# Optimization experiments

Measured on AMD Instinct MI355X. Metric: run time of the kernel, lower is better.

The kernel has to match this reference:

```python
import jax, jax.numpy as jnp
import numpy as np

B, N, D, H = 4, 4096, 1024, 16
DK = D // H  # 64


def setup_inputs() -> dict:
    key = jax.random.key(0)
    ks = jax.random.split(key, 11)
    s_in = 1.0 / np.sqrt(D)
    s_out = 1.0 / np.sqrt(H * DK)
    return {
        "query": jax.random.normal(ks[0], (B, N, D), jnp.float32),
        "key": jax.random.normal(ks[1], (B, N, D), jnp.float32),
        "value": jax.random.normal(ks[2], (B, N, D), jnp.float32),
        # stacked per-head Linear weights (torch Linear: y = x @ W.T + b)
        "Wq": jax.random.uniform(ks[3], (H, DK, D), jnp.float32, -s_in, s_in),
        "bq": jax.random.uniform(ks[4], (H, DK), jnp.float32, -s_in, s_in),
        "Wk": jax.random.uniform(ks[5], (H, DK, D), jnp.float32, -s_in, s_in),
        "bk": jax.random.uniform(ks[6], (H, DK), jnp.float32, -s_in, s_in),
        "Wv": jax.random.uniform(ks[7], (H, DK, D), jnp.float32, -s_in, s_in),
        "bv": jax.random.uniform(ks[8], (H, DK), jnp.float32, -s_in, s_in),
        "Wo": jax.random.uniform(ks[9], (D, H * DK), jnp.float32, -s_out, s_out),
        "bo": jax.random.uniform(ks[10], (D,), jnp.float32, -s_out, s_out),
    }


def reference(query, key, value, Wq, bq, Wk, bk, Wv, bv, Wo, bo):
    b, n, _ = query.shape
    # batched per-head projections: [b,h,n,d_k]
    q = jnp.einsum('bnd,hkd->bhnk', query, Wq) + bq[None, :, None, :]
    k = jnp.einsum('bnd,hkd->bhnk', key, Wk) + bk[None, :, None, :]
    v = jnp.einsum('bnd,hkd->bhnk', value, Wv) + bv[None, :, None, :]
    # linear dot-product attention (faithful: scale by batch**-0.5)
    q = jax.nn.softmax(q, axis=-1) * (b ** -0.5)
    k = jax.nn.softmax(k, axis=-2)  # softmax over sequence dim
    ctx = jnp.einsum('bhnd,bhne->bhde', k, v)      # [b,h,d_k,d_v]
    attn = jnp.einsum('bhnd,bhde->bhne', q, ctx)   # [b,h,n,d_v]
    # concat heads along last dim: [b,n,h*d_v]
    concat = attn.transpose(0, 2, 1, 3).reshape(b, n, -1)
    return concat @ Wo.T + bo
```

## Files before the change

### kernel.cpp

```cpp
#include <hip/hip_runtime.h>
#include <hip/hip_bf16.h>
#include <stdint.h>

#define B_  4
#define N_  4096
#define D_  1024
#define H_  16
#define DK_ 64
#define M_  (B_ * N_)

typedef __attribute__((ext_vector_type(8))) short  short8;
typedef __attribute__((ext_vector_type(4))) float  f32x4;
typedef __attribute__((ext_vector_type(4))) unsigned int u32x4;

__device__ __forceinline__ uint16_t f2bf(float f) {
  union { float f; uint32_t u; } v; v.f = f;
  uint32_t r = v.u + 0x7FFF + ((v.u >> 16) & 1);
  return (uint16_t)(r >> 16);
}
__device__ __forceinline__ uint32_t f2bf2(float lo, float hi) {
  return (uint32_t)f2bf(lo) | ((uint32_t)f2bf(hi) << 16);
}
__device__ __forceinline__ float bf2f(uint16_t u) {
  union { uint32_t u; float f; } v; v.u = ((uint32_t)u) << 16;
  return v.f;
}

__device__ __forceinline__ void gload_lds16(const void* g, void* l) {
  __builtin_amdgcn_global_load_lds((const __attribute__((address_space(1))) void*)g,
                                   (__attribute__((address_space(3))) void*)l, 16, 0, 0);
}

#define S_BARRIER() __builtin_amdgcn_s_barrier()
#define FENCE_LGKM0() asm volatile("s_waitcnt lgkmcnt(0)" ::: "memory")
#define FENCE_VM4()   asm volatile("s_waitcnt vmcnt(4) lgkmcnt(0)" ::: "memory")
#define FENCE_VM0()   asm volatile("s_waitcnt vmcnt(0) lgkmcnt(0)" ::: "memory")

__global__ __launch_bounds__(256) void pack_bf16_kernel(
    const float* q, const float* k, const float* v,
    const float* wq, const float* wk, const float* wv, const float* wo,
    uint16_t* xq, uint16_t* xk, uint16_t* xv,
    uint16_t* bwq, uint16_t* bwk, uint16_t* bwv, uint16_t* bwo)
{
  const float* src; uint16_t* dst; int count;
  switch (blockIdx.y) {
    case 0: src = q;  dst = xq;  count = M_ * D_; break;
    case 1: src = k;  dst = xk;  count = M_ * D_; break;
    case 2: src = v;  dst = xv;  count = M_ * D_; break;
    case 3: src = wq; dst = bwq; count = D_ * D_; break;
    case 4: src = wk; dst = bwk; count = D_ * D_; break;
    case 5: src = wv; dst = bwv; count = D_ * D_; break;
    default: src = wo; dst = bwo; count = D_ * D_; break;
  }
  int base = blockIdx.x * 16384;
  if (base >= count) return;
  int t = threadIdx.x;
#pragma unroll
  for (int it = 0; it < 8; ++it) {
    int idx = base + it * 2048 + t * 8;
    f32x4 f0 = *(const f32x4*)(src + idx);
    f32x4 f1 = *(const f32x4*)(src + idx + 4);
    u32x4 o;
    o.x = f2bf2(f0.x, f0.y); o.y = f2bf2(f0.z, f0.w);
    o.z = f2bf2(f1.x, f1.y); o.w = f2bf2(f1.z, f1.w);
    *(u32x4*)(dst + idx) = o;
  }
}

template<int EPI>
__device__ __forceinline__ void gemm_epilogue(
    f32x4 (&acc)[8][4], int tid, int l, int lr, int kg, int wr, int wc,
    int brow, int bcol, const float* __restrict__ bias, void* __restrict__ C,
    float* __restrict__ pm, float* __restrict__ ps,
    float* sredm, float* sreds)
{
  if (EPI == 2) {
    float bv[4];
#pragma unroll
    for (int ni = 0; ni < 4; ++ni) bv[ni] = bias[bcol * 256 + wc * 64 + ni * 16 + lr];
#pragma unroll
    for (int mi = 0; mi < 8; ++mi) {
#pragma unroll
      for (int j = 0; j < 4; ++j) {
        float v0 = acc[mi][0][j] + bv[0];
        float v1 = acc[mi][1][j] + bv[1];
        float v2 = acc[mi][2][j] + bv[2];
        float v3 = acc[mi][3][j] + bv[3];
        float m = fmaxf(fmaxf(v0, v1), fmaxf(v2, v3));
#pragma unroll
        for (int o = 1; o < 16; o <<= 1) m = fmaxf(m, __shfl_xor(m, o));
        float p0 = __expf(v0 - m), p1 = __expf(v1 - m);
        float p2 = __expf(v2 - m), p3 = __expf(v3 - m);
        float s = (p0 + p1) + (p2 + p3);
#pragma unroll
        for (int o = 1; o < 16; o <<= 1) s += __shfl_xor(s, o);
        float sc = 0.5f / s;
        int row = brow * 256 + wr * 128 + mi * 16 + kg * 4 + j;
        uint16_t* out = (uint16_t*)C + (size_t)row * D_ + bcol * 256 + wc * 64 + lr;
        out[0]  = f2bf(p0 * sc);
        out[16] = f2bf(p1 * sc);
        out[32] = f2bf(p2 * sc);
        out[48] = f2bf(p3 * sc);
      }
    }
  } else if (EPI == 3) {
#pragma unroll
    for (int ni = 0; ni < 4; ++ni) {
      int coll = wc * 64 + ni * 16 + lr;
      int col = bcol * 256 + coll;
      float bvn = bias[col];
      float vals[8][4];
      float m = -1e30f;
#pragma unroll
      for (int mi = 0; mi < 8; ++mi)
#pragma unroll
        for (int j = 0; j < 4; ++j) {
          float val = acc[mi][ni][j] + bvn;
          vals[mi][j] = val;
          m = fmaxf(m, val);
          int row = brow * 256 + wr * 128 + mi * 16 + kg * 4 + j;
          ((uint16_t*)C)[(size_t)row * D_ + col] = f2bf(val);
        }
      m = fmaxf(m, __shfl_xor(m, 16));
      m = fmaxf(m, __shfl_xor(m, 32));
      float s = 0.f;
#pragma unroll
      for (int mi = 0; mi < 8; ++mi)
#pragma unroll
        for (int j = 0; j < 4; ++j) s += __expf(vals[mi][j] - m);
      s += __shfl_xor(s, 16);
      s += __shfl_xor(s, 32);
      if (l < 16) {
        sredm[wr * 256 + coll] = m;
        sreds[wr * 256 + coll] = s;
      }
    }
    __syncthreads();
    if (tid < 256) {
      float m0 = sredm[tid], m1 = sredm[256 + tid];
      float s0 = sreds[tid], s1 = sreds[256 + tid];
      float m = fmaxf(m0, m1);
      float s = s0 * __expf(m0 - m) + s1 * __expf(m1 - m);
      pm[(size_t)brow * D_ + bcol * 256 + tid] = m;
      ps[(size_t)brow * D_ + bcol * 256 + tid] = s;
    }
  } else {
#pragma unroll
    for (int mi = 0; mi < 8; ++mi) {
#pragma unroll
      for (int ni = 0; ni < 4; ++ni) {
        int col = bcol * 256 + wc * 64 + ni * 16 + lr;
        float bv = bias[col];
#pragma unroll
        for (int j = 0; j < 4; ++j) {
          int row = brow * 256 + wr * 128 + mi * 16 + kg * 4 + j;
          float val = acc[mi][ni][j] + bv;
          if (EPI == 1) ((float*)C)[(size_t)row * D_ + col] = val;
          else          ((uint16_t*)C)[(size_t)row * D_ + col] = f2bf(val);
        }
      }
    }
  }
}

__device__ __forceinline__ void gemm256_body(
    const uint16_t* __restrict__ A, const uint16_t* __restrict__ Wb,
    uint16_t* As, uint16_t* Bs,
    int tid, int w, int arow0, int bcrow0, int srcswz, int rsw,
    int lr, int kg, int wr, int wc, f32x4 (&acc)[8][4])
{
  const int NT = 16;
  const uint16_t* gA[2][2];
  const uint16_t* gB[2][2];
  int lOff[2][2];
#pragma unroll
  for (int h = 0; h < 2; ++h)
#pragma unroll
    for (int i = 0; i < 2; ++i) {
      int lin = h * 16384 + i * 8192 + tid * 16;
      int src = lin ^ srcswz;
      size_t rowoff = (size_t)(src >> 7) * D_ + ((src & 127) >> 1);
      gA[h][i] = A + (size_t)arow0 * D_ + rowoff;
      gB[h][i] = Wb + (size_t)bcrow0 * D_ + rowoff;
      lOff[h][i] = h * 8192 + i * 4096 + w * 512;
    }
  auto stageA = [&](int kt, uint16_t* ldst, int h) {
    gload_lds16(gA[h][0] + kt * 64, ldst + lOff[h][0]);
    gload_lds16(gA[h][1] + kt * 64, ldst + lOff[h][1]);
  };
  auto stageB = [&](int kt, uint16_t* ldst, int h) {
    gload_lds16(gB[h][0] + kt * 64, ldst + lOff[h][0]);
    gload_lds16(gB[h][1] + kt * 64, ldst + lOff[h][1]);
  };
  auto rdfrag = [&](const uint16_t* tile, int row, int ks) -> short8 {
    return *(const short8*)(tile + row * 64 + ((((ks << 2) | kg) ^ rsw) << 3));
  };

  stageA(0, As, 0); stageA(0, As, 1);
  stageB(0, Bs, 0); stageB(0, Bs, 1);
  stageA(1, As + 16384, 0); stageA(1, As + 16384, 1);
  FENCE_VM4();
  S_BARRIER();

  short8 af0[4][2], af1[4][2], bfr[2][2];
  for (int t = 0; t < NT; ++t) {
    const int p = t & 1;
    uint16_t* Ap = As + p * 16384;
    uint16_t* Bp = Bs + p * 16384;
    uint16_t* Bn = Bs + (p ^ 1) * 16384;

#pragma unroll
    for (int mi = 0; mi < 4; ++mi)
#pragma unroll
      for (int ks = 0; ks < 2; ++ks)
        af0[mi][ks] = rdfrag(Ap, wr * 128 + mi * 16 + lr, ks);
#pragma unroll
    for (int ni = 0; ni < 2; ++ni)
#pragma unroll
      for (int ks = 0; ks < 2; ++ks)
        bfr[ni][ks] = rdfrag(Bp, wc * 64 + ni * 16 + lr, ks);
    if (t + 1 < NT) stageB(t + 1, Bn, 0);
    __builtin_amdgcn_s_setprio(1);
#pragma unroll
    for (int mi = 0; mi < 4; ++mi)
#pragma unroll
      for (int ni = 0; ni < 2; ++ni)
#pragma unroll
        for (int ks = 0; ks < 2; ++ks)
          acc[mi][ni] = __builtin_amdgcn_mfma_f32_16x16x32_bf16(af0[mi][ks], bfr[ni][ks], acc[mi][ni], 0, 0, 0);
    __builtin_amdgcn_s_setprio(0);
    FENCE_LGKM0();
    S_BARRIER();

#pragma unroll
    for (int mi = 0; mi < 4; ++mi)
#pragma unroll
      for (int ks = 0; ks < 2; ++ks)
        af1[mi][ks] = rdfrag(Ap, wr * 128 + 64 + mi * 16 + lr, ks);
    if (t + 1 < NT) stageB(t + 1, Bn, 1);
    __builtin_amdgcn_s_setprio(1);
#pragma unroll
    for (int mi = 0; mi < 4; ++mi)
#pragma unroll
      for (int ni = 0; ni < 2; ++ni)
#pragma unroll
        for (int ks = 0; ks < 2; ++ks)
          acc[mi + 4][ni] = __builtin_amdgcn_mfma_f32_16x16x32_bf16(af1[mi][ks], bfr[ni][ks], acc[mi + 4][ni], 0, 0, 0);
    __builtin_amdgcn_s_setprio(0);
    FENCE_LGKM0();
    S_BARRIER();

#pragma unroll
    for (int ni = 0; ni < 2; ++ni)
#pragma unroll
      for (int ks = 0; ks < 2; ++ks)
        bfr[ni][ks] = rdfrag(Bp, wc * 64 + (ni + 2) * 16 + lr, ks);
    if (t + 2 < NT) stageA(t + 2, Ap, 0);
    __builtin_amdgcn_s_setprio(1);
#pragma unroll
    for (int mi = 0; mi < 4; ++mi)
#pragma unroll
      for (int ni = 0; ni < 2; ++ni)
#pragma unroll
        for (int ks = 0; ks < 2; ++ks)
          acc[mi + 4][ni + 2] = __builtin_amdgcn_mfma_f32_16x16x32_bf16(af1[mi][ks], bfr[ni][ks], acc[mi + 4][ni + 2], 0, 0, 0);
    __builtin_amdgcn_s_setprio(0);
    FENCE_LGKM0();
    S_BARRIER();

    if (t + 2 < NT) stageA(t + 2, Ap, 1);
    __builtin_amdgcn_s_setprio(1);
#pragma unroll
    for (int mi = 0; mi < 4; ++mi)
#pragma unroll
      for (int ni = 0; ni < 2; ++ni)
#pragma unroll
        for (int ks = 0; ks < 2; ++ks)
          acc[mi][ni + 2] = __builtin_amdgcn_mfma_f32_16x16x32_bf16(af0[mi][ks], bfr[ni][ks], acc[mi][ni + 2], 0, 0, 0);
    __builtin_amdgcn_s_setprio(0);
    if (t <= 13)      { FENCE_VM4(); }
    else if (t == 14) { FENCE_VM0(); }
    else              { FENCE_LGKM0(); }
    S_BARRIER();
  }
}

__global__ __launch_bounds__(512, 2) void qkv_gemm256_kernel(
    const uint16_t* __restrict__ XQ, const uint16_t* __restrict__ XK,
    const uint16_t* __restrict__ XV,
    const uint16_t* __restrict__ WQ, const uint16_t* __restrict__ WK,
    const uint16_t* __restrict__ WV,
    const float* __restrict__ bq, const float* __restrict__ bk,
    const float* __restrict__ bv,
    uint16_t* __restrict__ QS, uint16_t* __restrict__ KP,
    uint16_t* __restrict__ VP,
    float* __restrict__ pm, float* __restrict__ ps)
{
  extern __shared__ uint16_t smem[];
  uint16_t* As = smem;
  uint16_t* Bs = smem + 32768;
  float* sredm = (float*)(smem + 65536);
  float* sreds = sredm + 512;

  const int tid = threadIdx.x;
  const int w = tid >> 6, l = tid & 63;
  const int lr = l & 15, kg = l >> 4;
  const int wr = w >> 2, wc = w & 3;
  const int rsw = lr & 7;
  const int srcswz = ((tid >> 3) & 7) << 4;

  const int flat = blockIdx.y * 4 + blockIdx.x;
  const int swzf = (flat & 7) * 32 + (flat >> 3);
  const int brow = swzf >> 2, bcol = swzf & 3;
  const int z = blockIdx.z;

  const uint16_t* A = (z == 0) ? XQ : (z == 1) ? XK : XV;
  const uint16_t* W = (z == 0) ? WQ : (z == 1) ? WK : WV;
  const float* bias = (z == 0) ? bq : (z == 1) ? bk : bv;
  void* C          = (z == 0) ? (void*)QS : (z == 1) ? (void*)KP : (void*)VP;

  f32x4 acc[8][4];
#pragma unroll
  for (int i = 0; i < 8; ++i)
#pragma unroll
    for (int j = 0; j < 4; ++j) acc[i][j] = (f32x4){0.f, 0.f, 0.f, 0.f};

  gemm256_body(A, W, As, Bs, tid, w, brow * 256, bcol * 256, srcswz, rsw,
               lr, kg, wr, wc, acc);

  if (z == 0)
    gemm_epilogue<2>(acc, tid, l, lr, kg, wr, wc, brow, bcol, bias, C, pm, ps, sredm, sreds);
  else if (z == 1)
    gemm_epilogue<3>(acc, tid, l, lr, kg, wr, wc, brow, bcol, bias, C, pm, ps, sredm, sreds);
  else
    gemm_epilogue<0>(acc, tid, l, lr, kg, wr, wc, brow, bcol, bias, C, pm, ps, sredm, sreds);
}

__global__ __launch_bounds__(512, 2) void gemm256_kernel(
    const uint16_t* __restrict__ A,
    const uint16_t* __restrict__ W,
    const float* __restrict__ bias,
    void* __restrict__ C)
{
  extern __shared__ uint16_t smem[];
  uint16_t* As = smem;
  uint16_t* Bs = smem + 32768;

  const int tid = threadIdx.x;
  const int w = tid >> 6, l = tid & 63;
  const int lr = l & 15, kg = l >> 4;
  const int wr = w >> 2, wc = w & 3;
  const int rsw = lr & 7;
  const int srcswz = ((tid >> 3) & 7) << 4;

  const int flat = blockIdx.y * 4 + blockIdx.x;
  const int swzf = (flat & 7) * 32 + (flat >> 3);
  const int brow = swzf >> 2, bcol = swzf & 3;

  const uint16_t* Wb = W + (size_t)(brow >> 4) * ((size_t)D_ * D_);

  f32x4 acc[8][4];
#pragma unroll
  for (int i = 0; i < 8; ++i)
#pragma unroll
    for (int j = 0; j < 4; ++j) acc[i][j] = (f32x4){0.f, 0.f, 0.f, 0.f};

  gemm256_body(A, Wb, As, Bs, tid, w, brow * 256, bcol * 256, srcswz, rsw,
               lr, kg, wr, wc, acc);

  gemm_epilogue<1>(acc, tid, l, lr, kg, wr, wc, brow, bcol, bias, C,
                   nullptr, nullptr, nullptr, nullptr);
}

__global__ __launch_bounds__(256) void ctx_partial_kernel(
    const uint16_t* __restrict__ kp, const uint16_t* __restrict__ vp,
    const float* __restrict__ pm, const float* __restrict__ ps,
    float* __restrict__ ctxp)
{
  __shared__ uint16_t wt[64][72];
  __shared__ uint16_t vt[64][72];
  __shared__ float cm[64], ci[64];
  const int t = threadIdx.x;
  const int w = t >> 6, l = t & 63;
  const int lr = l & 15, p = l >> 4;
  const int nchunk = blockIdx.x, h = blockIdx.y, b = blockIdx.z;
  if (t < 64) {
    int col = h * 64 + t;
    float m = -1e30f;
#pragma unroll 4
    for (int c = 0; c < 16; ++c)
      m = fmaxf(m, pm[(size_t)(b * 16 + c) * D_ + col]);
    float s = 0.f;
#pragma unroll 4
    for (int c = 0; c < 16; ++c)
      s += ps[(size_t)(b * 16 + c) * D_ + col] * __expf(pm[(size_t)(b * 16 + c) * D_ + col] - m);
    cm[t] = m;
    ci[t] = 1.f / s;
  }
  __syncthreads();

  f32x4 acc[4];
#pragma unroll
  for (int i = 0; i < 4; ++i) acc[i] = (f32x4){0.f, 0.f, 0.f, 0.f};

  for (int tt = 0; tt < 8; ++tt) {
    int n0 = nchunk * 512 + tt * 64;
#pragma unroll
    for (int i = 0; i < 4; ++i) {
      int r = i * 16 + w * 4 + p;
      int c4 = lr * 4;
      size_t gi = (size_t)(b * N_ + n0 + r) * D_ + h * 64 + c4;
      union { uint16_t s[4]; uint2 u; } kk, vv;
      kk.u = *(const uint2*)(kp + gi);
      vv.u = *(const uint2*)(vp + gi);
      float a0 = __expf(bf2f(kk.s[0]) - cm[c4 + 0]) * ci[c4 + 0];
      float a1 = __expf(bf2f(kk.s[1]) - cm[c4 + 1]) * ci[c4 + 1];
      float a2 = __expf(bf2f(kk.s[2]) - cm[c4 + 2]) * ci[c4 + 2];
      float a3 = __expf(bf2f(kk.s[3]) - cm[c4 + 3]) * ci[c4 + 3];
      float s0 = __shfl_xor(a0, 16), s1 = __shfl_xor(a1, 16);
      float s2 = __shfl_xor(a2, 16), s3 = __shfl_xor(a3, 16);
      float c0 = (p & 1) ? s1 : a0, c1 = (p & 1) ? a1 : s0;
      float c2 = (p & 1) ? s3 : a2, c3 = (p & 1) ? a3 : s2;
      float S0 = __shfl_xor(c0, 32), S1 = __shfl_xor(c1, 32);
      float S2 = __shfl_xor(c2, 32), S3 = __shfl_xor(c3, 32);
      float e0 = (p & 2) ? S2 : c0, e1 = (p & 2) ? S3 : c1;
      float e2 = (p & 2) ? c2 : S0, e3 = (p & 2) ? c3 : S1;
      int rbase = i * 16 + w * 4;
      int cc = lr * 4 + p;
      *(uint2*)&wt[cc][rbase] = make_uint2(f2bf2(e0, e1), f2bf2(e2, e3));
      int b0 = vv.s[0], b1 = vv.s[1], b2 = vv.s[2], b3 = vv.s[3];
      int t0 = __shfl_xor(b0, 16), t1 = __shfl_xor(b1, 16);
      int t2 = __shfl_xor(b2, 16), t3 = __shfl_xor(b3, 16);
      int d0 = (p & 1) ? t1 : b0, d1 = (p & 1) ? b1 : t0;
      int d2 = (p & 1) ? t3 : b2, d3 = (p & 1) ? b3 : t2;
      int T0 = __shfl_xor(d0, 32), T1 = __shfl_xor(d1, 32);
      int T2 = __shfl_xor(d2, 32), T3 = __shfl_xor(d3, 32);
      uint32_t f0 = (p & 2) ? T2 : d0, f1 = (p & 2) ? T3 : d1;
      uint32_t f2v = (p & 2) ? d2 : T0, f3 = (p & 2) ? d3 : T1;
      *(uint2*)&vt[cc][rbase] =
          make_uint2((f0 & 0xFFFFu) | (f1 << 16), (f2v & 0xFFFFu) | (f3 << 16));
    }
    __syncthreads();
    short8 af[2];
#pragma unroll
    for (int ks = 0; ks < 2; ++ks)
      af[ks] = *(const short8*)(&wt[w * 16 + lr][ks * 32 + p * 8]);
#pragma unroll
    for (int ni = 0; ni < 4; ++ni)
#pragma unroll
      for (int ks = 0; ks < 2; ++ks) {
        short8 bfv = *(const short8*)(&vt[ni * 16 + lr][ks * 32 + p * 8]);
        acc[ni] = __builtin_amdgcn_mfma_f32_16x16x32_bf16(af[ks], bfv, acc[ni], 0, 0, 0);
      }
    __syncthreads();
  }
  float* out = ctxp + (size_t)(nchunk * 64 + b * 16 + h) * 4096;
#pragma unroll
  for (int ni = 0; ni < 4; ++ni)
#pragma unroll
    for (int j = 0; j < 4; ++j)
      out[(w * 16 + p * 4 + j) * 64 + ni * 16 + lr] = acc[ni][j];
}

__global__ __launch_bounds__(256) void ctx_reduce_kernel(
    const float* __restrict__ ctxp, float* __restrict__ ctx)
{
  int o = (blockIdx.x * 256 + threadIdx.x) * 4;
  f32x4 s = (f32x4){0.f, 0.f, 0.f, 0.f};
  for (int c = 0; c < 8; ++c) s = s + *(const f32x4*)(ctxp + (size_t)c * 262144 + o);
  *(f32x4*)(ctx + o) = s;
}

__global__ __launch_bounds__(256) void w2t_kernel(
    const float* __restrict__ ctx,
    const uint16_t* __restrict__ wo,
    uint16_t* __restrict__ w2t)
{
  __shared__ float ctxL[64][65];
  __shared__ float woL[64][65];
  int t = threadIdx.x;
  int otile = blockIdx.x, h = blockIdx.y, b = blockIdx.z;
  const float* csrc = ctx + (size_t)(b * 16 + h) * 4096;
#pragma unroll
  for (int i = 0; i < 4; ++i) {
    int idx = (i * 256 + t) * 4;
    int r = idx >> 6, c = idx & 63;
    f32x4 cv = *(const f32x4*)(csrc + idx);
    union { uint16_t s[4]; uint2 u; } wv;
    wv.u = *(const uint2*)(wo + (size_t)(otile * 64 + r) * D_ + h * 64 + c);
#pragma unroll
    for (int j = 0; j < 4; ++j) {
      ctxL[r][c + j] = cv[j];
      woL[r][c + j] = bf2f(wv.s[j]);
    }
  }
  __syncthreads();
  int ol = (t & 15) * 4, dl = (t >> 4) * 4;
  float acc[4][4];
#pragma unroll
  for (int i = 0; i < 4; ++i)
#pragma unroll
    for (int j = 0; j < 4; ++j) acc[i][j] = 0.f;
#pragma unroll 4
  for (int e = 0; e < 64; ++e) {
    float cv[4], wv[4];
#pragma unroll
    for (int i = 0; i < 4; ++i) { cv[i] = ctxL[dl + i][e]; wv[i] = woL[ol + i][e]; }
#pragma unroll
    for (int di = 0; di < 4; ++di)
#pragma unroll
      for (int oi = 0; oi < 4; ++oi) acc[di][oi] += cv[di] * wv[oi];
  }
  uint16_t* dst = w2t + (size_t)b * D_ * D_ + (size_t)(otile * 64) * D_ + h * 64;
#pragma unroll
  for (int oi = 0; oi < 4; ++oi) {
    union { uint16_t s[4]; uint2 u; } o4;
#pragma unroll
    for (int di = 0; di < 4; ++di) o4.s[di] = f2bf(acc[di][oi]);
    *(uint2*)(dst + (size_t)(ol + oi) * D_ + dl) = o4.u;
  }
}

extern "C" void kernel_launch(void* const* d_in, const int* in_sizes, int n_in,
                              void* d_out, int out_size, void* d_ws, size_t ws_size,
                              hipStream_t stream)
{
  const float* q  = (const float*)d_in[0];
  const float* k  = (const float*)d_in[1];
  const float* v  = (const float*)d_in[2];
  const float* Wq = (const float*)d_in[3];
  const float* bq = (const float*)d_in[4];
  const float* Wk = (const float*)d_in[5];
  const float* bk = (const float*)d_in[6];
  const float* Wv = (const float*)d_in[7];
  const float* bv = (const float*)d_in[8];
  const float* Wo = (const float*)d_in[9];
  const float* bo = (const float*)d_in[10];

  char* ws = (char*)d_ws;
  const size_t XB = (size_t)M_ * D_ * 2;
  const size_t WB = (size_t)D_ * D_ * 2;
  uint16_t* XQ  = (uint16_t*)(ws);
  uint16_t* XK  = (uint16_t*)(ws + XB);
  uint16_t* XV  = (uint16_t*)(ws + 2 * XB);
  uint16_t* WQb = (uint16_t*)(ws + 3 * XB);
  uint16_t* WKb = (uint16_t*)(ws + 3 * XB + WB);
  uint16_t* WVb = (uint16_t*)(ws + 3 * XB + 2 * WB);
  uint16_t* WOb = (uint16_t*)(ws + 3 * XB + 3 * WB);
  uint16_t* QS  = (uint16_t*)(ws + 3 * XB + 4 * WB);
  uint16_t* KP  = (uint16_t*)(ws + 4 * XB + 4 * WB);
  uint16_t* VP  = (uint16_t*)(ws + 5 * XB + 4 * WB);
  float* pm = (float*)d_out;
  float* ps = (float*)((char*)d_out + (256 << 10));
  float* ctxp = (float*)((char*)XK + (1 << 20));
  float* ctx  = (float*)((char*)XK + (9 << 20));
  uint16_t* W2T = XQ;

  const size_t LDSB = 135168;

  pack_bf16_kernel<<<dim3(1024, 7), 256, 0, stream>>>(
      q, k, v, Wq, Wk, Wv, Wo, XQ, XK, XV, WQb, WKb, WVb, WOb);

  qkv_gemm256_kernel<<<dim3(4, 64, 3), 512, LDSB, stream>>>(
      XQ, XK, XV, WQb, WKb, WVb, bq, bk, bv, QS, KP, VP, pm, ps);

  ctx_partial_kernel<<<dim3(8, H_, B_), 256, 0, stream>>>(KP, VP, pm, ps, ctxp);
  ctx_reduce_kernel<<<256, 256, 0, stream>>>(ctxp, ctx);

  w2t_kernel<<<dim3(16, 16, 4), 256, 0, stream>>>(ctx, WOb, W2T);

  gemm256_kernel<<<dim3(4, 64), 512, LDSB, stream>>>(QS, W2T, bo, d_out);
}
```

Before: 259.6 us.

## Fuse fp32-to-bf16 activation conversion into QKV GEMM A-tile loads

```diff
diff --git a/kernel.cpp b/kernel.cpp
--- a/kernel.cpp
+++ b/kernel.cpp
@@ -36,28 +36,22 @@
 #define FENCE_VM4()   asm volatile("s_waitcnt vmcnt(4) lgkmcnt(0)" ::: "memory")
 #define FENCE_VM0()   asm volatile("s_waitcnt vmcnt(0) lgkmcnt(0)" ::: "memory")
 
-__global__ __launch_bounds__(256) void pack_bf16_kernel(
-    const float* q, const float* k, const float* v,
+__global__ __launch_bounds__(256) void packw_kernel(
     const float* wq, const float* wk, const float* wv, const float* wo,
-    uint16_t* xq, uint16_t* xk, uint16_t* xv,
     uint16_t* bwq, uint16_t* bwk, uint16_t* bwv, uint16_t* bwo)
 {
-  const float* src; uint16_t* dst; int count;
+  const float* src; uint16_t* dst;
   switch (blockIdx.y) {
-    case 0: src = q;  dst = xq;  count = M_ * D_; break;
-    case 1: src = k;  dst = xk;  count = M_ * D_; break;
-    case 2: src = v;  dst = xv;  count = M_ * D_; break;
-    case 3: src = wq; dst = bwq; count = D_ * D_; break;
-    case 4: src = wk; dst = bwk; count = D_ * D_; break;
-    case 5: src = wv; dst = bwv; count = D_ * D_; break;
-    default: src = wo; dst = bwo; count = D_ * D_; break;
-  }
-  int base = blockIdx.x * 16384;
-  if (base >= count) return;
+    case 0: src = wq; dst = bwq; break;
+    case 1: src = wk; dst = bwk; break;
+    case 2: src = wv; dst = bwv; break;
+    default: src = wo; dst = bwo; break;
+  }
+  int base = blockIdx.x * 4096;
   int t = threadIdx.x;
 #pragma unroll
-  for (int it = 0; it < 8; ++it) {
-    int idx = base + it * 2048 + t * 8;
+  for (int j = 0; j < 2; ++j) {
+    int idx = base + j * 2048 + t * 8;
     f32x4 f0 = *(const f32x4*)(src + idx);
     f32x4 f1 = *(const f32x4*)(src + idx + 4);
     u32x4 o;
@@ -160,6 +154,149 @@
         }
       }
     }
+  }
+}
+
+__device__ __forceinline__ void gemm256f_body(
+    const float* __restrict__ A, const uint16_t* __restrict__ Wb,
+    char* Af, uint16_t* Bs,
+    int tid, int w, int arow0, int bcrow0, int l,
+    int lr, int kg, int wr, int wc, f32x4 (&acc)[8][4])
+{
+  const int NT = 16;
+  const int rsw = lr & 7;
+  const float* gA[8]; int lOffA[8];
+  const uint16_t* gB[2][2]; int lOffB[2][2];
+#pragma unroll
+  for (int i = 0; i < 8; ++i) {
+    int lin = i * 8192 + tid * 16;
+    int src = lin ^ (((lin >> 8) & 7) << 4);
+    gA[i] = A + (size_t)(arow0 + (src >> 8)) * D_ + ((src & 255) >> 2);
+    lOffA[i] = i * 8192 + w * 1024;
+  }
+  const int srcswzB = ((tid >> 3) & 7) << 4;
+#pragma unroll
+  for (int h = 0; h < 2; ++h)
+#pragma unroll
+    for (int i = 0; i < 2; ++i) {
+      int lin = h * 16384 + i * 8192 + tid * 16;
+      int src = lin ^ srcswzB;
+      gB[h][i] = Wb + (size_t)(bcrow0 + (src >> 7)) * D_ + ((src & 127) >> 1);
+      lOffB[h][i] = h * 8192 + i * 4096 + w * 512;
+    }
+  auto stageAh = [&](int kt, int h) {
+#pragma unroll
+    for (int i = 0; i < 4; ++i) {
+      int j = h * 4 + i;
+      gload_lds16(gA[j] + kt * 64, Af + lOffA[j]);
+    }
+  };
+  auto stageB = [&](int kt, uint16_t* ldst) {
+#pragma unroll
+    for (int h = 0; h < 2; ++h)
+#pragma unroll
+      for (int i = 0; i < 2; ++i)
+        gload_lds16(gB[h][i] + kt * 64, ldst + lOffB[h][i]);
+  };
+  auto rdfragA = [&](int row, int ks) -> short8 {
+    int base = row * 256 + ks * 128 + kg * 32;
+    int sw = (row & 7) << 4;
+    f32x4 x0 = *(const f32x4*)(Af + ((base + 0)  ^ sw));
+    f32x4 x1 = *(const f32x4*)(Af + ((base + 16) ^ sw));
+    union { uint32_t u[4]; short8 s; } r;
+    asm("v_cvt_pk_bf16_f32 %0, %1, %2" : "=v"(r.u[0]) : "v"(x0.x), "v"(x0.y));
+    asm("v_cvt_pk_bf16_f32 %0, %1, %2" : "=v"(r.u[1]) : "v"(x0.z), "v"(x0.w));
+    asm("v_cvt_pk_bf16_f32 %0, %1, %2" : "=v"(r.u[2]) : "v"(x1.x), "v"(x1.y));
+    asm("v_cvt_pk_bf16_f32 %0, %1, %2" : "=v"(r.u[3]) : "v"(x1.z), "v"(x1.w));
+    return r.s;
+  };
+  auto rdfragB = [&](const uint16_t* tile, int row, int ks) -> short8 {
+    return *(const short8*)(tile + row * 64 + ((((ks << 2) | kg) ^ rsw) << 3));
+  };
+
+  stageAh(0, 0); stageAh(0, 1);
+  stageB(0, Bs);
+  stageB(1, Bs + 16384);
+  FENCE_VM4();
+  S_BARRIER();
+
+  short8 af0[4][2], af1[4][2], bfr[2][2];
+  for (int t = 0; t < NT; ++t) {
+    const int p = t & 1;
+    uint16_t* Bp = Bs + p * 16384;
+
+#pragma unroll
+    for (int mi = 0; mi < 4; ++mi)
+#pragma unroll
+      for (int ks = 0; ks < 2; ++ks)
+        af0[mi][ks] = rdfragA(wr * 128 + mi * 16 + lr, ks);
+#pragma unroll
+    for (int ni = 0; ni < 2; ++ni)
+#pragma unroll
+      for (int ks = 0; ks < 2; ++ks)
+        bfr[ni][ks] = rdfragB(Bp, wc * 64 + ni * 16 + lr, ks);
+    __builtin_amdgcn_s_setprio(1);
+#pragma unroll
+    for (int mi = 0; mi < 4; ++mi)
+#pragma unroll
+      for (int ni = 0; ni < 2; ++ni)
+#pragma unroll
+        for (int ks = 0; ks < 2; ++ks)
+          acc[mi][ni] = __builtin_amdgcn_mfma_f32_16x16x32_bf16(af0[mi][ks], bfr[ni][ks], acc[mi][ni], 0, 0, 0);
+    __builtin_amdgcn_s_setprio(0);
+    FENCE_LGKM0();
+    S_BARRIER();
+
+#pragma unroll
+    for (int mi = 0; mi < 4; ++mi)
+#pragma unroll
+      for (int ks = 0; ks < 2; ++ks)
+        af1[mi][ks] = rdfragA(wr * 128 + 64 + mi * 16 + lr, ks);
+    __builtin_amdgcn_s_setprio(1);
+#pragma unroll
+    for (int mi = 0; mi < 4; ++mi)
+#pragma unroll
+      for (int ni = 0; ni < 2; ++ni)
+#pragma unroll
+        for (int ks = 0; ks < 2; ++ks)
+          acc[mi + 4][ni] = __builtin_amdgcn_mfma_f32_16x16x32_bf16(af1[mi][ks], bfr[ni][ks], acc[mi + 4][ni], 0, 0, 0);
+    __builtin_amdgcn_s_setprio(0);
+    FENCE_LGKM0();
+    S_BARRIER();
+
+#pragma unroll
+    for (int ni = 0; ni < 2; ++ni)
+#pragma unroll
+      for (int ks = 0; ks < 2; ++ks)
+        bfr[ni][ks] = rdfragB(Bp, wc * 64 + (ni + 2) * 16 + lr, ks);
+    if (t + 1 < NT) stageAh(t + 1, 0);
+    __builtin_amdgcn_s_setprio(1);
+#pragma unroll
+    for (int mi = 0; mi < 4; ++mi)
+#pragma unroll
+      for (int ni = 0; ni < 2; ++ni)
+#pragma unroll
+        for (int ks = 0; ks < 2; ++ks)
+          acc[mi + 4][ni + 2] = __builtin_amdgcn_mfma_f32_16x16x32_bf16(af1[mi][ks], bfr[ni][ks], acc[mi + 4][ni + 2], 0, 0, 0);
+    __builtin_amdgcn_s_setprio(0);
+    FENCE_LGKM0();
+    S_BARRIER();
+
+    if (t + 1 < NT) stageAh(t + 1, 1);
+    if (t + 2 < NT) stageB(t + 2, Bs + p * 16384);
+    __builtin_amdgcn_s_setprio(1);
+#pragma unroll
+    for (int mi = 0; mi < 4; ++mi)
+#pragma unroll
+      for (int ni = 0; ni < 2; ++ni)
+#pragma unroll
+        for (int ks = 0; ks < 2; ++ks)
+          acc[mi][ni + 2] = __builtin_amdgcn_mfma_f32_16x16x32_bf16(af0[mi][ks], bfr[ni][ks], acc[mi][ni + 2], 0, 0, 0);
+    __builtin_amdgcn_s_setprio(0);
+    if (t <= 13)      { FENCE_VM4(); }
+    else if (t == 14) { FENCE_VM0(); }
+    else              { FENCE_LGKM0(); }
+    S_BARRIER();
   }
 }
 
@@ -285,9 +422,9 @@
   }
 }
 
-__global__ __launch_bounds__(512, 2) void qkv_gemm256_kernel(
-    const uint16_t* __restrict__ XQ, const uint16_t* __restrict__ XK,
-    const uint16_t* __restrict__ XV,
+__global__ __launch_bounds__(512, 2) void qkv_gemm256f_kernel(
+    const float* __restrict__ q, const float* __restrict__ k,
+    const float* __restrict__ v,
     const uint16_t* __restrict__ WQ, const uint16_t* __restrict__ WK,
     const uint16_t* __restrict__ WV,
     const float* __restrict__ bq, const float* __restrict__ bk,
@@ -296,28 +433,25 @@
     uint16_t* __restrict__ VP,
     float* __restrict__ pm, float* __restrict__ ps)
 {
-  extern __shared__ uint16_t smem[];
-  uint16_t* As = smem;
-  uint16_t* Bs = smem + 32768;
-  float* sredm = (float*)(smem + 65536);
+  extern __shared__ char smemf[];
+  char* Af = smemf;
+  uint16_t* Bs = (uint16_t*)(smemf + 65536);
+  float* sredm = (float*)(smemf + 131072);
   float* sreds = sredm + 512;
 
   const int tid = threadIdx.x;
   const int w = tid >> 6, l = tid & 63;
   const int lr = l & 15, kg = l >> 4;
   const int wr = w >> 2, wc = w & 3;
-  const int rsw = lr & 7;
-  const int srcswz = ((tid >> 3) & 7) << 4;
-
   const int flat = blockIdx.y * 4 + blockIdx.x;
   const int swzf = (flat & 7) * 32 + (flat >> 3);
   const int brow = swzf >> 2, bcol = swzf & 3;
   const int z = blockIdx.z;
 
-  const uint16_t* A = (z == 0) ? XQ : (z == 1) ? XK : XV;
-  const uint16_t* W = (z == 0) ? WQ : (z == 1) ? WK : WV;
-  const float* bias = (z == 0) ? bq : (z == 1) ? bk : bv;
-  void* C          = (z == 0) ? (void*)QS : (z == 1) ? (void*)KP : (void*)VP;
+  const float* A     = (z == 0) ? q  : (z == 1) ? k  : v;
+  const uint16_t* W  = (z == 0) ? WQ : (z == 1) ? WK : WV;
+  const float* bias  = (z == 0) ? bq : (z == 1) ? bk : bv;
+  void* C            = (z == 0) ? (void*)QS : (z == 1) ? (void*)KP : (void*)VP;
 
   f32x4 acc[8][4];
 #pragma unroll
@@ -325,8 +459,8 @@
 #pragma unroll
     for (int j = 0; j < 4; ++j) acc[i][j] = (f32x4){0.f, 0.f, 0.f, 0.f};
 
-  gemm256_body(A, W, As, Bs, tid, w, brow * 256, bcol * 256, srcswz, rsw,
-               lr, kg, wr, wc, acc);
+  gemm256f_body(A, W, Af, Bs, tid, w, brow * 256, bcol * 256, l,
+                lr, kg, wr, wc, acc);
 
   if (z == 0)
     gemm_epilogue<2>(acc, tid, l, lr, kg, wr, wc, brow, bcol, bias, C, pm, ps, sredm, sreds);
@@ -538,31 +672,27 @@
   const float* bo = (const float*)d_in[10];
 
   char* ws = (char*)d_ws;
-  const size_t XB = (size_t)M_ * D_ * 2;
-  const size_t WB = (size_t)D_ * D_ * 2;
-  uint16_t* XQ  = (uint16_t*)(ws);
-  uint16_t* XK  = (uint16_t*)(ws + XB);
-  uint16_t* XV  = (uint16_t*)(ws + 2 * XB);
-  uint16_t* WQb = (uint16_t*)(ws + 3 * XB);
-  uint16_t* WKb = (uint16_t*)(ws + 3 * XB + WB);
-  uint16_t* WVb = (uint16_t*)(ws + 3 * XB + 2 * WB);
-  uint16_t* WOb = (uint16_t*)(ws + 3 * XB + 3 * WB);
-  uint16_t* QS  = (uint16_t*)(ws + 3 * XB + 4 * WB);
-  uint16_t* KP  = (uint16_t*)(ws + 4 * XB + 4 * WB);
-  uint16_t* VP  = (uint16_t*)(ws + 5 * XB + 4 * WB);
+  const size_t MB = 1 << 20;
+  uint16_t* WQb = (uint16_t*)(ws);
+  uint16_t* WKb = (uint16_t*)(ws + 2 * MB);
+  uint16_t* WVb = (uint16_t*)(ws + 4 * MB);
+  uint16_t* WOb = (uint16_t*)(ws + 6 * MB);
+  uint16_t* QS  = (uint16_t*)(ws + 8 * MB);
+  uint16_t* KP  = (uint16_t*)(ws + 40 * MB);
+  uint16_t* VP  = (uint16_t*)(ws + 72 * MB);
+  uint16_t* W2T = (uint16_t*)(ws + 104 * MB);
+  float* ctxp   = (float*)(ws + 112 * MB);
+  float* ctx    = (float*)(ws + 120 * MB);
   float* pm = (float*)d_out;
   float* ps = (float*)((char*)d_out + (256 << 10));
-  float* ctxp = (float*)((char*)XK + (1 << 20));
-  float* ctx  = (float*)((char*)XK + (9 << 20));
-  uint16_t* W2T = XQ;
 
   const size_t LDSB = 135168;
 
-  pack_bf16_kernel<<<dim3(1024, 7), 256, 0, stream>>>(
-      q, k, v, Wq, Wk, Wv, Wo, XQ, XK, XV, WQb, WKb, WVb, WOb);
-
-  qkv_gemm256_kernel<<<dim3(4, 64, 3), 512, LDSB, stream>>>(
-      XQ, XK, XV, WQb, WKb, WVb, bq, bk, bv, QS, KP, VP, pm, ps);
+  packw_kernel<<<dim3(256, 4), 256, 0, stream>>>(
+      Wq, Wk, Wv, Wo, WQb, WKb, WVb, WOb);
+
+  qkv_gemm256f_kernel<<<dim3(4, 64, 3), 512, LDSB, stream>>>(
+      q, k, v, WQb, WKb, WVb, bq, bk, bv, QS, KP, VP, pm, ps);
 
   ctx_partial_kernel<<<dim3(8, H_, B_), 256, 0, stream>>>(KP, VP, pm, ps, ctxp);
   ctx_reduce_kernel<<<256, 256, 0, stream>>>(ctxp, ctx);
```

Result: slower. 777.7 us (+199.6%).
